# Kernel optimization log

Measured on AMD Instinct MI355X. Metric: run time of the kernel, lower is better.

## Reference

```python
import jax, jax.numpy as jnp
import numpy as np
from jax import lax

NUM_LABELS = 64  # groundtruth labels in [0, 64); label 0 = background (ignored in pair counts)


def _edges(H, W):
    # channel 0: edge (i,j)-(i+1,j); channel 1: edge (i,j)-(i,j+1)
    idx = np.arange(H * W).reshape(H, W)
    u0 = idx.copy(); v0 = np.roll(idx, -1, axis=0)
    u0[-1, :] = 0; v0[-1, :] = 0  # invalid boundary edges -> self edge, no-op
    u1 = idx.copy(); v1 = np.roll(idx, -1, axis=1)
    u1[:, -1] = 0; v1[:, -1] = 0
    u = np.concatenate([u0.ravel(), u1.ravel()]).astype(np.int32)
    v = np.concatenate([v0.ravel(), v1.ravel()]).astype(np.int32)
    return jnp.asarray(u), jnp.asarray(v)


def _find(parent, x, iters):
    # union-by-size keeps tree depth <= log2(N)+1, so a fixed number of hops suffices
    return lax.fori_loop(0, iters, lambda i, p: parent[p], x)


def _npairs(order, u, v, labels, pos):
    """Kruskal over edges sorted by descending affinity; for each merging edge,
    count pairs of voxels for which it is the maximin edge (pos: same nonzero
    label; neg: different nonzero labels). Pure int computation (non-diff)."""
    N = labels.shape[0]
    iters = int(np.ceil(np.log2(N))) + 2
    parent0 = jnp.arange(N, dtype=jnp.int32)
    size0 = jnp.ones(N, jnp.int32)
    counts0 = jax.nn.one_hot(labels, NUM_LABELS, dtype=jnp.int32)  # [N, L] label histogram per root

    def step(carry, e):
        parent, size, counts = carry
        ru = _find(parent, u[e], iters)
        rv = _find(parent, v[e], iters)
        cu = counts[ru]; cv = counts[rv]
        same = jnp.dot(cu[1:], cv[1:])          # same-nonzero-label pairs
        tu = cu[1:].sum(); tv = cv[1:].sum()    # nonzero-label voxel counts
        n = same if pos else tu * tv - same     # differing-label pairs for neg pass
        merge = ru != rv
        n = jnp.where(merge, n, 0)
        big = jnp.where(size[ru] >= size[rv], ru, rv)
        small = ru + rv - big
        parent = parent.at[small].set(jnp.where(merge, big, parent[small]))
        size = size.at[big].add(jnp.where(merge, size[small], 0))
        counts = counts.at[big].add(jnp.where(merge, counts[small], 0))
        return (parent, size, counts), n

    _, n = lax.scan(step, (parent0, size0, counts0), order)
    return n  # [E] int32, aligned with sorted order


def _malis_grad(aff, labels, u, v):
    # aff [E] float, labels [N] int. MALIS pseudo-loss gradients:
    # pos pass grad_e = n_pos_e * (a_e - 1); neg pass grad_e = n_neg_e * a_e;
    # combined = -(pos + neg) / 2 (as in MalisLoss.forward).
    order = jnp.argsort(-lax.stop_gradient(aff)).astype(jnp.int32)
    a_sorted = aff[order]
    n_pos = _npairs(order, u, v, labels, True).astype(aff.dtype)
    n_neg = _npairs(order, u, v, labels, False).astype(aff.dtype)
    g_sorted = n_pos * (a_sorted - 1.0) + n_neg * a_sorted
    return jnp.zeros_like(aff).at[order].set(-0.5 * g_sorted)


def setup_inputs() -> dict:
    key = jax.random.key(0)
    k1, k2 = jax.random.split(key)
    affinities = jax.random.uniform(k1, (2, 2, 128, 128), dtype=jnp.float32)
    groundtruth = jax.random.randint(k2, (2, 128, 128), 0, NUM_LABELS, dtype=jnp.int64)
    return {"affinities": affinities, "groundtruth": groundtruth}


def reference(affinities, groundtruth):
    B, C, H, W = affinities.shape
    u, v = _edges(H, W)
    aff = affinities.reshape(B, C * H * W)
    lab = groundtruth.reshape(B, H * W).astype(jnp.int32)
    grads = jax.vmap(lambda a, l: _malis_grad(a, l, u, v))(aff, lab)
    return grads.sum()  # pseudo_loss
```

## Files before the change

### kernel.cpp

```cpp
#include <hip/hip_runtime.h>

#define HDIM 128
#define WDIM 128
#define NPIX (HDIM * WDIM)
#define NEDGE (2 * NPIX)
#define BANDS 128

typedef unsigned long long ull;

__device__ __forceinline__ void decode_edge(unsigned e, int& u, int& v) {
  if (e >= (unsigned)NEDGE) { u = 0; v = 0; return; }
  if (e < NPIX) {
    if (e < NPIX - WDIM) { u = (int)e; v = (int)e + WDIM; } else { u = 0; v = 0; }
  } else {
    unsigned t2 = e - NPIX;
    if ((t2 & (WDIM - 1)) != (WDIM - 1)) { u = (int)t2; v = (int)t2 + 1; } else { u = 0; v = 0; }
  }
}

__device__ __forceinline__ int bucket_of(float a) {
  int f = (int)(a * 128.0f);
  f = f < 0 ? 0 : (f > 127 ? 127 : f);
  return 127 - f;
}

__device__ __forceinline__ int cc_find(volatile unsigned* p, int x) {
  int px = (int)p[x];
  while (px != x) {
    int g = (int)p[px];
    if (g != px) p[x] = (unsigned)g;
    x = px; px = g;
  }
  return x;
}

__device__ __forceinline__ void uf_find2(unsigned* pn, int x, int y,
                                         int& rx, int& ry,
                                         unsigned& nzx, unsigned& nzy) {
  unsigned wx = pn[x];
  unsigned wy = pn[y];
  while (true) {
    int px = (int)(wx & 0xFFFFu);
    int py = (int)(wy & 0xFFFFu);
    bool mx = (px != x);
    bool my = (py != y);
    if (!mx && !my) break;
    if (mx) {
      unsigned wpx = pn[px];
      int gx = (int)(wpx & 0xFFFFu);
      if (gx != px) { pn[x] = (wx & 0xFFFF0000u) | (unsigned)gx; x = gx; wx = pn[gx]; }
      else { x = px; wx = wpx; }
    }
    if (my) {
      unsigned wpy = pn[py];
      int gy = (int)(wpy & 0xFFFFu);
      if (gy != py) { pn[y] = (wy & 0xFFFF0000u) | (unsigned)gy; y = gy; wy = pn[gy]; }
      else { y = py; wy = wpy; }
    }
  }
  rx = x; ry = y; nzx = wx >> 16; nzy = wy >> 16;
}

__global__ __launch_bounds__(1024) void band_kernel(const int* __restrict__ gt,
                                                    const float* __restrict__ aff_g,
                                                    float* __restrict__ out) {
  __shared__ unsigned pn[NPIX];
  const int img = blockIdx.x / BANDS, band = blockIdx.x % BANDS;
  const int* lab = gt + (size_t)img * NPIX;
  const float* aff = aff_g + (size_t)img * NEDGE;
  const int tid = threadIdx.x;

  if (band == 0) {
    if (tid < 64) pn[tid] = 0;
    __syncthreads();
    for (int i = tid; i < NPIX; i += 1024) atomicAdd(&pn[(unsigned)lab[i] & 63u], 1u);
    __syncthreads();
    if (tid == 0) {
      double s = 0.0;
      for (int l = 1; l < 64; ++l) { double m = (double)pn[l]; s += m * (m - 1.0) * 0.5; }
      atomicAdd(out, (float)(0.5 * s));
    }
    __syncthreads();
  }

  ull* sk = (ull*)pn;
  unsigned* scnt = &pn[2047];
  if (tid == 0) *scnt = 0;
  __syncthreads();
  for (int e = tid; e < NEDGE; e += 1024) {
    float a = aff[e];
    if (bucket_of(a) != band) continue;
    int u, v; decode_edge((unsigned)e, u, v);
    if (u == v) continue;
    unsigned bits = __float_as_uint(a);
    unsigned ob = (bits & 0x80000000u) ? ~bits : (bits | 0x80000000u);
    unsigned pos = atomicAdd(scnt, 1u);
    if (pos < 512u) sk[pos] = ((ull)(~ob) << 32) | (unsigned)e;
  }
  __syncthreads();
  unsigned cnt = *scnt; if (cnt > 512u) cnt = 512u;

  unsigned npow2 = 64; while (npow2 < cnt) npow2 <<= 1;
  for (unsigned i = tid; i < npow2; i += 1024) if (i >= cnt) sk[i] = ~0ull;
  __syncthreads();
  for (unsigned k = 2; k <= npow2; k <<= 1) {
    for (unsigned j = k >> 1; j > 0; j >>= 1) {
      for (unsigned t = tid; t < npow2; t += 1024) {
        unsigned ixj = t ^ j;
        if (ixj > t) {
          bool up = ((t & k) == 0);
          ull a0 = sk[t], a1 = sk[ixj];
          if ((a0 > a1) == up) { sk[t] = a1; sk[ixj] = a0; }
        }
      }
      __syncthreads();
    }
  }
  ull myk[8];
  if (tid < 64) {
#pragma unroll
    for (int b8 = 0; b8 < 8; ++b8) {
      unsigned idx = (unsigned)(b8 * 64) + (unsigned)tid;
      myk[b8] = (idx < npow2) ? sk[idx] : ~0ull;
    }
  }
  __syncthreads();

  for (int i = tid; i < NPIX; i += 1024) pn[i] = (unsigned)i;
  __syncthreads();
  volatile unsigned* vp = pn;
  for (int e = tid; e < NEDGE; e += 1024) {
    if (bucket_of(aff[e]) >= band) continue;
    int u, v; decode_edge((unsigned)e, u, v);
    if (u == v) continue;
    while (true) {
      int ru = cc_find(vp, u), rv = cc_find(vp, v);
      if (ru == rv) break;
      if (ru < rv) { int t = ru; ru = rv; rv = t; }
      unsigned old = atomicCAS(&pn[ru], (unsigned)ru, (unsigned)rv);
      if (old == (unsigned)ru) break;
      u = ru; v = rv;
    }
  }
  __syncthreads();

  {
    const int i0 = tid << 4;
    int prev = -1; unsigned acc = 0;
    for (int k = 0; k < 16; ++k) {
      int i = i0 + k;
      int r = i; unsigned p;
      while (((p = vp[r]) & 0xFFFFu) != (unsigned)r) r = (int)(p & 0xFFFFu);
      if (i != r) pn[i] = (unsigned)r;
      unsigned c = (lab[i] != 0) ? 1u : 0u;
      if (r != prev) {
        if (acc) atomicAdd(&pn[prev], acc << 16);
        prev = r; acc = c;
      } else {
        acc += c;
      }
    }
    if (acc) atomicAdd(&pn[prev], acc << 16);
  }
  __syncthreads();

  if (tid < 64) {
    const int lane = tid;
    double acc = 0.0;
#pragma unroll
    for (int b8 = 0; b8 < 8; ++b8) {
      if ((unsigned)(b8 * 64) >= cnt) break;
      const ull myk_b = myk[b8];
      unsigned e = (unsigned)myk_b;
      unsigned khi = (unsigned)(myk_b >> 32);
      int u, v; decode_edge(e, u, v);
      const bool valid = (u != v);
      unsigned ob = ~khi;
      unsigned bits = (ob & 0x80000000u) ? (ob & 0x7FFFFFFFu) : ~ob;
      const float a = __uint_as_float(bits);

      int ru, rv; unsigned nzu, nzv;
      uf_find2(pn, u, v, ru, rv, nzu, nzv);

      unsigned long long m = __ballot(valid && (ru != rv));
      int myW = 0, myL = 0; unsigned snap = 0;
      while (m) {
        const int j = (int)(__ffsll(m) - 1);
        m &= m - 1;
        const int ruj = __builtin_amdgcn_readlane(ru, j);
        const int rvj = __builtin_amdgcn_readlane(rv, j);
        const unsigned nzuj = (unsigned)__builtin_amdgcn_readlane((int)nzu, j);
        const unsigned nzvj = (unsigned)__builtin_amdgcn_readlane((int)nzv, j);
        const bool live = (ruj != rvj);
        const unsigned mnz = nzuj + nzvj;
        int W = (nzuj >= nzvj) ? ruj : rvj;
        int L = ruj + rvj - W;
        W = live ? W : -1;
        L = live ? L : -1;
        const int sj = live ? j : 64;
        const unsigned spk = nzuj | (nzvj << 16);
        const bool turn = (lane == sj);
        if (turn) { myW = W; myL = L; snap = spk; }
        const bool uW = (ru == W), uL = (ru == L);
        const bool vW = (rv == W), vL = (rv == L);
        if (uL) ru = W;
        if (uW | uL) nzu = mnz;
        if (vL) rv = W;
        if (vW | vL) nzv = mnz;
      }
      pn[u] = (unsigned)ru;
      pn[v] = (unsigned)rv;
      if (myW != myL) {
        pn[myL] = (unsigned)myW;
        acc += (double)((snap & 0xFFFFu) * (snap >> 16)) * (double)a;
      }
      pn[ru] = (nzu << 16) | (unsigned)ru;
      pn[rv] = (nzv << 16) | (unsigned)rv;
    }
    for (int off = 32; off > 0; off >>= 1) acc += __shfl_down(acc, off);
    if (lane == 0) atomicAdd(out, (float)(-0.5 * acc));
  }
}

extern "C" void kernel_launch(void* const* d_in, const int* in_sizes, int n_in,
                              void* d_out, int out_size, void* d_ws, size_t ws_size,
                              hipStream_t stream) {
  const float* aff = (const float*)d_in[0];
  const int* gt = (const int*)d_in[1];
  float* out = (float*)d_out;
  const int B = in_sizes[1] / NPIX;

  hipMemsetAsync(d_out, 0, sizeof(float) * (size_t)out_size, stream);
  band_kernel<<<dim3(B * BANDS), dim3(1024), 0, stream>>>(gt, aff, out);
}
```

Baseline: 147.5 us.

## Fuse edge scan with union-find and overlap wave-level sort with root compression

Merges the band-edge collection pass and the lower-band connected-component union pass into one sweep over the affinities, so the global reads happen once and one barrier phase disappears. The 512-key bitonic sort moves from a block-wide shared-memory sort with a barrier per stage into a single wavefront using registers and cross-lane shuffles. That sort runs while the other 15 wavefronts do path compression and nonzero-label counting. The counting also switches to a strided pixel assignment, with a wave-level reduction when a whole wave lands on one root. The risks are a longer serial sort on one wave, less coalesced strided pixel access, and more CAS contention while the collection work is interleaved.

Result: faster. 132.6 us (-10.1%).

```diff
diff --git a/kernel.cpp b/kernel.cpp
--- a/kernel.cpp
+++ b/kernel.cpp
@@ -5,6 +5,7 @@
 #define NPIX (HDIM * WDIM)
 #define NEDGE (2 * NPIX)
 #define BANDS 128
+#define MAXK 512
 
 typedef unsigned long long ull;
 
@@ -61,10 +62,18 @@
   rx = x; ry = y; nzx = wx >> 16; nzy = wy >> 16;
 }
 
+__device__ __forceinline__ ull shflx64(ull x, int m) {
+  int lo = __shfl_xor((int)(unsigned)x, m, 64);
+  int hi = __shfl_xor((int)(unsigned)(x >> 32), m, 64);
+  return ((ull)(unsigned)hi << 32) | (unsigned)lo;
+}
+
 __global__ __launch_bounds__(1024) void band_kernel(const int* __restrict__ gt,
                                                     const float* __restrict__ aff_g,
                                                     float* __restrict__ out) {
   __shared__ unsigned pn[NPIX];
+  __shared__ ull skbuf[MAXK];
+  __shared__ unsigned scnt;
   const int img = blockIdx.x / BANDS, band = blockIdx.x % BANDS;
   const int* lab = gt + (size_t)img * NPIX;
   const float* aff = aff_g + (size_t)img * NEDGE;
@@ -83,84 +92,99 @@
     __syncthreads();
   }
 
-  ull* sk = (ull*)pn;
-  unsigned* scnt = &pn[2047];
-  if (tid == 0) *scnt = 0;
+  for (int i = tid; i < NPIX; i += 1024) pn[i] = (unsigned)i;
+  if (tid == 0) scnt = 0;
   __syncthreads();
+
+  volatile unsigned* vp = pn;
   for (int e = tid; e < NEDGE; e += 1024) {
     float a = aff[e];
-    if (bucket_of(a) != band) continue;
+    int b = bucket_of(a);
+    if (b > band) continue;
     int u, v; decode_edge((unsigned)e, u, v);
     if (u == v) continue;
-    unsigned bits = __float_as_uint(a);
-    unsigned ob = (bits & 0x80000000u) ? ~bits : (bits | 0x80000000u);
-    unsigned pos = atomicAdd(scnt, 1u);
-    if (pos < 512u) sk[pos] = ((ull)(~ob) << 32) | (unsigned)e;
+    if (b == band) {
+      unsigned bits = __float_as_uint(a);
+      unsigned ob = (bits & 0x80000000u) ? ~bits : (bits | 0x80000000u);
+      unsigned pos = atomicAdd(&scnt, 1u);
+      if (pos < MAXK) skbuf[pos] = ((ull)(~ob) << 32) | (unsigned)e;
+    } else {
+      while (true) {
+        int ru = cc_find(vp, u), rv = cc_find(vp, v);
+        if (ru == rv) break;
+        if (ru < rv) { int t = ru; ru = rv; rv = t; }
+        unsigned old = atomicCAS(&pn[ru], (unsigned)ru, (unsigned)rv);
+        if (old == (unsigned)ru) break;
+        u = ru; v = rv;
+      }
+    }
   }
   __syncthreads();
-  unsigned cnt = *scnt; if (cnt > 512u) cnt = 512u;
-
-  unsigned npow2 = 64; while (npow2 < cnt) npow2 <<= 1;
-  for (unsigned i = tid; i < npow2; i += 1024) if (i >= cnt) sk[i] = ~0ull;
-  __syncthreads();
-  for (unsigned k = 2; k <= npow2; k <<= 1) {
-    for (unsigned j = k >> 1; j > 0; j >>= 1) {
-      for (unsigned t = tid; t < npow2; t += 1024) {
-        unsigned ixj = t ^ j;
-        if (ixj > t) {
-          bool up = ((t & k) == 0);
-          ull a0 = sk[t], a1 = sk[ixj];
-          if ((a0 > a1) == up) { sk[t] = a1; sk[ixj] = a0; }
+  unsigned cnt = scnt; if (cnt > MAXK) cnt = MAXK;
+
+  ull myv[8];
+  if (tid < 64) {
+    const int lane = tid;
+#pragma unroll
+    for (int r = 0; r < 8; ++r) {
+      unsigned idx = (unsigned)(r * 64 + lane);
+      myv[r] = (idx < cnt) ? skbuf[idx] : ~0ull;
+    }
+#pragma unroll
+    for (unsigned k = 2; k <= 512; k <<= 1) {
+#pragma unroll
+      for (unsigned j = k >> 1; j; j >>= 1) {
+        if (j >= 64) {
+          const int rj = (int)(j >> 6);
+#pragma unroll
+          for (int r = 0; r < 8; ++r) {
+            if (!(r & rj)) {
+              const int p = r | rj;
+              const bool dir = ((((unsigned)r << 6) & k) == 0);
+              ull a0 = myv[r], a1 = myv[p];
+              if ((a0 > a1) == dir) { myv[r] = a1; myv[p] = a0; }
+            }
+          }
+        } else {
+#pragma unroll
+          for (int r = 0; r < 8; ++r) {
+            ull pv = shflx64(myv[r], (int)j);
+            const bool low = ((lane & (int)j) == 0);
+            const bool dir = (((((unsigned)r << 6) | (unsigned)lane) & k) == 0);
+            const bool takemin = (low == dir);
+            const bool less = (myv[r] < pv);
+            myv[r] = (less == takemin) ? myv[r] : pv;
+          }
         }
       }
-      __syncthreads();
-    }
-  }
-  ull myk[8];
-  if (tid < 64) {
-#pragma unroll
-    for (int b8 = 0; b8 < 8; ++b8) {
-      unsigned idx = (unsigned)(b8 * 64) + (unsigned)tid;
-      myk[b8] = (idx < npow2) ? sk[idx] : ~0ull;
-    }
-  }
-  __syncthreads();
-
-  for (int i = tid; i < NPIX; i += 1024) pn[i] = (unsigned)i;
-  __syncthreads();
-  volatile unsigned* vp = pn;
-  for (int e = tid; e < NEDGE; e += 1024) {
-    if (bucket_of(aff[e]) >= band) continue;
-    int u, v; decode_edge((unsigned)e, u, v);
-    if (u == v) continue;
-    while (true) {
-      int ru = cc_find(vp, u), rv = cc_find(vp, v);
-      if (ru == rv) break;
-      if (ru < rv) { int t = ru; ru = rv; rv = t; }
-      unsigned old = atomicCAS(&pn[ru], (unsigned)ru, (unsigned)rv);
-      if (old == (unsigned)ru) break;
-      u = ru; v = rv;
-    }
-  }
-  __syncthreads();
-
-  {
-    const int i0 = tid << 4;
-    int prev = -1; unsigned acc = 0;
-    for (int k = 0; k < 16; ++k) {
-      int i = i0 + k;
+    }
+  } else {
+    const int t = tid - 64;
+    int prev = -1; unsigned acc = 0; bool multi = false;
+    for (int k = 0; k < 18; ++k) {
+      int i = t + k * 960;
+      if (i >= NPIX) break;
       int r = i; unsigned p;
       while (((p = vp[r]) & 0xFFFFu) != (unsigned)r) r = (int)(p & 0xFFFFu);
       if (i != r) pn[i] = (unsigned)r;
       unsigned c = (lab[i] != 0) ? 1u : 0u;
       if (r != prev) {
-        if (acc) atomicAdd(&pn[prev], acc << 16);
+        if (prev >= 0) { if (acc) atomicAdd(&pn[prev], acc << 16); multi = true; }
         prev = r; acc = c;
       } else {
         acc += c;
       }
     }
-    if (acc) atomicAdd(&pn[prev], acc << 16);
+    const int wl = tid & 63;
+    int first = __shfl(prev, 0);
+    bool uni = __all(!multi && prev == first);
+    if (uni) {
+      unsigned s = acc;
+      for (int off = 32; off; off >>= 1) s += __shfl_down(s, off);
+      if (wl == 0 && s) atomicAdd(&pn[prev], s << 16);
+    } else if (acc) {
+      atomicAdd(&pn[prev], acc << 16);
+    }
   }
   __syncthreads();
 
@@ -170,7 +194,7 @@
 #pragma unroll
     for (int b8 = 0; b8 < 8; ++b8) {
       if ((unsigned)(b8 * 64) >= cnt) break;
-      const ull myk_b = myk[b8];
+      const ull myk_b = myv[b8];
       unsigned e = (unsigned)myk_b;
       unsigned khi = (unsigned)(myk_b >> 32);
       int u, v; decode_edge(e, u, v);
```
